# Kernel optimization log

Hardware: AMD Instinct MI355X
Metric: run time of the kernel (lower is better)

The kernel has to match this reference:

```python
import jax, jax.numpy as jnp
import numpy as np

B, G, NIN, H = 4, 1200, 10, 4
NHE, NINC = 300, 4800
ALPHA, BETA = 0.005, 5e-5
BN_EPS = 1e-5


def _linear_init(key, out_d, in_d):
    s = 1.0 / np.sqrt(in_d)
    kw, kb = jax.random.split(key)
    w = jax.random.uniform(kw, (out_d, in_d), jnp.float32, -s, s)
    b = jax.random.uniform(kb, (out_d,), jnp.float32, -s, s)
    return w, b


def setup_inputs() -> dict:
    key = jax.random.key(0)
    ks = jax.random.split(key, 16)
    d = {}
    d['x'] = jax.random.normal(ks[0], (B, G, NIN), jnp.float32)
    d['edge1'] = (jax.random.uniform(ks[1], (G, G)) < 0.02).astype(jnp.float32)
    d['edge2'] = (jax.random.uniform(ks[2], (G, G)) < 0.02).astype(jnp.float32)
    d['W1'] = jax.random.normal(ks[3], (G, G), jnp.float32) / np.sqrt(G)
    d['b1'] = jax.random.uniform(ks[4], (G,), jnp.float32)
    d['infer_w'], d['infer_b'] = _linear_init(ks[5], H, NIN)
    d['mlp_e1_w'], d['mlp_e1_b'] = _linear_init(ks[6], 1, 2 * H)
    d['mlp_e2_w'], d['mlp_e2_b'] = _linear_init(ks[7], 1, 2 * H)
    d['nodes1_w'], d['nodes1_b'] = _linear_init(ks[8], H, 2 * H)
    d['nodes2_w'], d['nodes2_b'] = _linear_init(ks[9], H, 2 * H)
    d['mm1_w'], d['mm1_b'] = _linear_init(ks[10], H, 2 * H)
    d['mm2_w'], d['mm2_b'] = _linear_init(ks[11], H, 2 * H)
    d['mm3_w'], d['mm3_b'] = _linear_init(ks[12], H, 2 * H)
    d['hg_w'], d['hg_b'] = _linear_init(ks[13], H, H)
    d['hyper_nodes'] = jax.random.randint(ks[14], (NINC,), 0, G)
    d['hyper_edges'] = jax.random.randint(ks[15], (NINC,), 0, NHE)
    return d


def _bn(y):
    # BatchNorm1d(gene_num) in train mode, gamma=1 beta=0: normalize per gene over (batch, feat)
    m = y.mean(axis=(0, 2), keepdims=True)
    v = y.var(axis=(0, 2), keepdims=True)
    return (y - m) * jax.lax.rsqrt(v + BN_EPS)


def _round(x, edge, coef, ew, eb, nw, nb, mw, mb):
    # one-hot matmul gather == repeat/tile; flat edge k = i*G + j, i=target, j=source
    Bsz, Gn, Hd = x.shape
    xi = jnp.repeat(x, Gn, axis=1)            # x[:, k // G]  (node_shape1 @ x)
    xj = jnp.tile(x, (1, Gn, 1))              # x[:, k %  G]  (node_shape2 @ x)
    ef = jnp.concatenate([xj, xi], axis=-1)   # [B, G*G, 2H]
    gate = jax.nn.sigmoid(ef @ ew.T + eb)     # [B, G*G, 1]
    mask = (edge + coef * (edge == 0).astype(x.dtype)).reshape(1, Gn * Gn, 1)
    msg = ef * (gate * mask)
    # transpose-matmul scatter back to target node i == sum over j
    recv = msg.reshape(Bsz, Gn, Gn, 2 * Hd).sum(axis=2)
    recv = jax.nn.elu(recv @ nw.T + nb)
    return jax.nn.elu(jnp.concatenate([recv, x], axis=-1) @ mw.T + mb)


def _forward(x, edge1, edge2, W1, b1, infer_w, infer_b, mlp_e1_w, mlp_e1_b,
             mlp_e2_w, mlp_e2_b, nodes1_w, nodes1_b, nodes2_w, nodes2_b,
             mm1_w, mm1_b, mm2_w, mm2_b, mm3_w, mm3_b, hg_w, hg_b,
             hyper_nodes, hyper_edges):
    Bsz, Gn, _ = x.shape
    h = jax.nn.elu(x @ infer_w.T + infer_b)                      # [B, G, H]
    upd = _round(h, edge1, ALPHA, mlp_e1_w, mlp_e1_b, nodes1_w, nodes1_b, mm1_w, mm1_b)
    # F.linear with w1 = eye(G) * W1 is a per-gene diagonal scale + per-gene bias
    h = jax.nn.elu(upd * jnp.diag(W1)[None, :, None] + b1[None, :, None])
    h = _bn(h)
    upd2 = _bn(_round(h, edge2, BETA, mlp_e2_w, mlp_e2_b, nodes2_w, nodes2_b, mm2_w, mm2_b))
    # HypergraphConv (PyG): out = D^-1 H (B^-1 H^T (X W)) + b.  Source overwrites the
    # hyper_graph1 result, so only hyper_graph2 contributes to the output.
    xf = upd2.reshape(Bsz * Gn, -1) @ hg_w.T
    node_idx = (hyper_nodes[None, :] + jnp.arange(Bsz)[:, None] * Gn).reshape(-1)
    edge_idx = jnp.tile(hyper_edges, Bsz)    # hyperedge ids NOT offset per batch (source quirk)
    nn_tot = Bsz * Gn
    ones = jnp.ones(node_idx.shape, xf.dtype)
    deg = jax.ops.segment_sum(ones, node_idx, num_segments=nn_tot)
    dinv = jnp.where(deg > 0, 1.0 / deg, 0.0)
    bdeg = jax.ops.segment_sum(ones, edge_idx, num_segments=NHE)
    binv = jnp.where(bdeg > 0, 1.0 / bdeg, 0.0)
    efeat = binv[:, None] * jax.ops.segment_sum(xf[node_idx], edge_idx, num_segments=NHE)
    hx = dinv[:, None] * jax.ops.segment_sum(efeat[edge_idx], node_idx, num_segments=nn_tot)
    hx = jax.nn.elu(hx + hg_b).reshape(Bsz, Gn, -1)
    return jax.nn.elu(jnp.concatenate([upd2, hx], axis=-1) @ mm3_w.T + mm3_b)


def reference(x, edge1, edge2, W1, b1, infer_w, infer_b, mlp_e1_w, mlp_e1_b,
              mlp_e2_w, mlp_e2_b, nodes1_w, nodes1_b, nodes2_w, nodes2_b,
              mm1_w, mm1_b, mm2_w, mm2_b, mm3_w, mm3_b, hg_w, hg_b,
              hyper_nodes, hyper_edges):
    return _forward(x, edge1, edge2, W1, b1, infer_w, infer_b, mlp_e1_w, mlp_e1_b,
                    mlp_e2_w, mlp_e2_b, nodes1_w, nodes1_b, nodes2_w, nodes2_b,
                    mm1_w, mm1_b, mm2_w, mm2_b, mm3_w, mm3_b, hg_w, hg_b,
                    hyper_nodes, hyper_edges)
```

## Files before the change

kernel.cpp:

```cpp
#include <hip/hip_runtime.h>
#include <math.h>

#define G 1200
#define BSZ 4
#define NIN 10
#define NHE 300
#define NINC 4800
#define ALPHA 0.005f
#define BETA 5e-5f
#define BN_EPS 1e-5f

__device__ __forceinline__ float eluf(float x) { return x > 0.f ? x : __expf(x) - 1.f; }
__device__ __forceinline__ float sigf(float x) { return 1.f / (1.f + __expf(-x)); }

__global__ __launch_bounds__(256)
void infer_kernel(const float* __restrict__ x,
                  const float* __restrict__ infer_w, const float* __restrict__ infer_b,
                  const float* __restrict__ e1w, const float* __restrict__ e1b,
                  float4* __restrict__ xfeat1, float* __restrict__ a1, float* __restrict__ c1,
                  int* __restrict__ zero_region ) {
    if (blockIdx.x == 0) {
        for (int t = threadIdx.x; t < NHE * 4 + NHE * 0 + 1200 + 300 - 1200; t += 256) {}
        for (int t = threadIdx.x; t < 1500; t += 256) zero_region[t] = 0;
    }
    int n = blockIdx.x * blockDim.x + threadIdx.x;
    if (n >= BSZ * G) return;
    const float* xp = x + n * NIN;
    float h[4];
#pragma unroll
    for (int f = 0; f < 4; ++f) {
        float s = infer_b[f];
#pragma unroll
        for (int k = 0; k < NIN; ++k) s += infer_w[f * NIN + k] * xp[k];
        h[f] = eluf(s);
    }
    xfeat1[n] = make_float4(h[0], h[1], h[2], h[3]);
    float av = 0.f, cv = 0.f;
#pragma unroll
    for (int f = 0; f < 4; ++f) { av += e1w[f] * h[f]; cv += e1w[4 + f] * h[f]; }
    a1[n] = av;
    c1[n] = cv + e1b[0];
}

template <int MODE>
__global__ __launch_bounds__(256)
void round_kernel(const float* __restrict__ edge, float coef,
                  const float4* __restrict__ xfeat,
                  const float* __restrict__ a, const float* __restrict__ c,
                  const float* __restrict__ nw, const float* __restrict__ nb,
                  const float* __restrict__ mw, const float* __restrict__ mb,
                  const float* __restrict__ W1, const float* __restrict__ b1,
                  const float* __restrict__ gw, const float* __restrict__ gb,
                  const float* __restrict__ hgw,
                  float4* __restrict__ out_feat,
                  float* __restrict__ a_out, float* __restrict__ c_out,
                  const int* __restrict__ hn, const int* __restrict__ he,
                  float* __restrict__ efeat_g, int* __restrict__ eh_g,
                  int* __restrict__ deg_g) {
    const int i = blockIdx.x;
    const int tid = threadIdx.x;
    const int lane = tid & 63;
    const int w = tid >> 6;
    const float* erow = edge + (size_t)i * G;

    const float cb = c[w * G + i];
    float acc0 = 0.f, acc1 = 0.f, acc2 = 0.f, acc3 = 0.f, acc4 = 0.f;

    for (int j = lane; j < G; j += 64) {
        float m = erow[j];
        float mask = (m == 0.f) ? coef : m;
        float4 xj = xfeat[w * G + j];
        float s = sigf(a[w * G + j] + cb) * mask;
        acc0 += s * xj.x;
        acc1 += s * xj.y;
        acc2 += s * xj.z;
        acc3 += s * xj.w;
        acc4 += s;
    }
#pragma unroll
    for (int o = 32; o > 0; o >>= 1) {
        acc0 += __shfl_down(acc0, o, 64);
        acc1 += __shfl_down(acc1, o, 64);
        acc2 += __shfl_down(acc2, o, 64);
        acc3 += __shfl_down(acc3, o, 64);
        acc4 += __shfl_down(acc4, o, 64);
    }

    __shared__ float t[4][5];
    __shared__ float hvs[4][4];
    __shared__ float stats[2];
    __shared__ float bss[4][4];
    __shared__ float bsf[4];
    __shared__ int degs;

    if (lane == 0) {
        t[w][0] = acc0; t[w][1] = acc1; t[w][2] = acc2; t[w][3] = acc3; t[w][4] = acc4;
    }
    if (tid == 0) degs = 0;
    __syncthreads();

    if (tid < 4) {
        const int b = tid;
        float4 xi4 = xfeat[b * G + i];
        float xi[4] = {xi4.x, xi4.y, xi4.z, xi4.w};
        float ssum = t[b][4];
        float r8[8];
#pragma unroll
        for (int k = 0; k < 4; ++k) { r8[k] = t[b][k]; r8[4 + k] = xi[k] * ssum; }
        float r[4];
#pragma unroll
        for (int f = 0; f < 4; ++f) {
            float s = nb[f];
#pragma unroll
            for (int k = 0; k < 8; ++k) s += nw[f * 8 + k] * r8[k];
            r[f] = eluf(s);
        }
        float w1d = 0.f, b1i = 0.f;
        if (MODE == 1) { w1d = W1[(size_t)i * G + i]; b1i = b1[i]; }
#pragma unroll
        for (int f = 0; f < 4; ++f) {
            float s = mb[f];
#pragma unroll
            for (int k = 0; k < 4; ++k) s += mw[f * 8 + k] * r[k] + mw[f * 8 + 4 + k] * xi[k];
            float z = eluf(s);
            hvs[b][f] = (MODE == 1) ? eluf(z * w1d + b1i) : z;
        }
    }
    __syncthreads();

    if (tid == 0) {
        float mean = 0.f;
#pragma unroll
        for (int b = 0; b < 4; ++b)
#pragma unroll
            for (int f = 0; f < 4; ++f) mean += hvs[b][f];
        mean *= (1.f / 16.f);
        float var = 0.f;
#pragma unroll
        for (int b = 0; b < 4; ++b)
#pragma unroll
            for (int f = 0; f < 4; ++f) { float d = hvs[b][f] - mean; var += d * d; }
        var *= (1.f / 16.f);
        stats[0] = mean;
        stats[1] = rsqrtf(var + BN_EPS);
    }
    __syncthreads();

    if (tid < 4) {
        const int b = tid;
        const float mean = stats[0], sc = stats[1];
        float hv[4];
#pragma unroll
        for (int f = 0; f < 4; ++f) hv[f] = (hvs[b][f] - mean) * sc;
        out_feat[b * G + i] = make_float4(hv[0], hv[1], hv[2], hv[3]);
        if (MODE == 1) {
            float av = 0.f, cv = 0.f;
#pragma unroll
            for (int f = 0; f < 4; ++f) { av += gw[f] * hv[f]; cv += gw[4 + f] * hv[f]; }
            a_out[b * G + i] = av;
            c_out[b * G + i] = cv + gb[0];
        } else {
#pragma unroll
            for (int f = 0; f < 4; ++f) {
                float s = 0.f;
#pragma unroll
                for (int k = 0; k < 4; ++k) s += hgw[f * 4 + k] * hv[k];
                bss[b][f] = s;
            }
        }
    }

    if (MODE == 2) {
        __syncthreads();
        if (tid < 4) bsf[tid] = bss[0][tid] + bss[1][tid] + bss[2][tid] + bss[3][tid];
        __syncthreads();
        const float b0 = bsf[0], b1v = bsf[1], b2 = bsf[2], b3 = bsf[3];
        int cnt = 0;
        for (int cI = tid; cI < NINC; cI += 256) {
            if (hn[cI] == i) {
                ++cnt;
                int e = he[cI];
                atomicAdd(&eh_g[e], 1);
                atomicAdd(&efeat_g[e * 4 + 0], b0);
                atomicAdd(&efeat_g[e * 4 + 1], b1v);
                atomicAdd(&efeat_g[e * 4 + 2], b2);
                atomicAdd(&efeat_g[e * 4 + 3], b3);
            }
        }
        if (cnt) atomicAdd(&degs, cnt);
        __syncthreads();
        if (tid == 0) deg_g[i] = degs;
    }
}

__global__ __launch_bounds__(256)
void final_kernel(const int* __restrict__ hn, const int* __restrict__ he,
                  const float* __restrict__ efeat_g, const int* __restrict__ eh_g,
                  const int* __restrict__ deg_g,
                  const float4* __restrict__ upd2, const float* __restrict__ hgb,
                  const float* __restrict__ m3w, const float* __restrict__ m3b,
                  float4* __restrict__ out) {
    const int i = blockIdx.x;
    const int tid = threadIdx.x;
    const int lane = tid & 63;
    const int w = tid >> 6;

    float a0 = 0.f, a1 = 0.f, a2 = 0.f, a3 = 0.f;
    for (int cI = tid; cI < NINC; cI += 256) {
        if (hn[cI] == i) {
            int e = he[cI];
            float binv = 0.25f / (float)eh_g[e];
            a0 += efeat_g[e * 4 + 0] * binv;
            a1 += efeat_g[e * 4 + 1] * binv;
            a2 += efeat_g[e * 4 + 2] * binv;
            a3 += efeat_g[e * 4 + 3] * binv;
        }
    }
#pragma unroll
    for (int o = 32; o > 0; o >>= 1) {
        a0 += __shfl_down(a0, o, 64);
        a1 += __shfl_down(a1, o, 64);
        a2 += __shfl_down(a2, o, 64);
        a3 += __shfl_down(a3, o, 64);
    }
    __shared__ float red[4][4];
    if (lane == 0) { red[w][0] = a0; red[w][1] = a1; red[w][2] = a2; red[w][3] = a3; }
    __syncthreads();

    if (tid < 4) {
        const int b = tid;
        int dg = deg_g[i];
        float dinv = dg > 0 ? 1.f / (float)dg : 0.f;
        float hxp[4];
#pragma unroll
        for (int f = 0; f < 4; ++f) {
            float hx = (red[0][f] + red[1][f] + red[2][f] + red[3][f]) * dinv;
            hxp[f] = eluf(hx + hgb[f]);
        }
        float4 u4 = upd2[b * G + i];
        float u[4] = {u4.x, u4.y, u4.z, u4.w};
        float o4[4];
#pragma unroll
        for (int f = 0; f < 4; ++f) {
            float s = m3b[f];
#pragma unroll
            for (int k = 0; k < 4; ++k) s += m3w[f * 8 + k] * u[k] + m3w[f * 8 + 4 + k] * hxp[k];
            o4[f] = eluf(s);
        }
        out[b * G + i] = make_float4(o4[0], o4[1], o4[2], o4[3]);
    }
}

extern "C" void kernel_launch(void* const* d_in, const int* in_sizes, int n_in,
                              void* d_out, int out_size, void* d_ws, size_t ws_size,
                              hipStream_t stream) {
    const float* x       = (const float*)d_in[0];
    const float* edge1   = (const float*)d_in[1];
    const float* edge2   = (const float*)d_in[2];
    const float* W1      = (const float*)d_in[3];
    const float* b1      = (const float*)d_in[4];
    const float* infer_w = (const float*)d_in[5];
    const float* infer_b = (const float*)d_in[6];
    const float* e1w     = (const float*)d_in[7];
    const float* e1b     = (const float*)d_in[8];
    const float* e2w     = (const float*)d_in[9];
    const float* e2b     = (const float*)d_in[10];
    const float* n1w     = (const float*)d_in[11];
    const float* n1b     = (const float*)d_in[12];
    const float* n2w     = (const float*)d_in[13];
    const float* n2b     = (const float*)d_in[14];
    const float* m1w     = (const float*)d_in[15];
    const float* m1b     = (const float*)d_in[16];
    const float* m2w     = (const float*)d_in[17];
    const float* m2b     = (const float*)d_in[18];
    const float* m3w     = (const float*)d_in[19];
    const float* m3b     = (const float*)d_in[20];
    const float* hgw     = (const float*)d_in[21];
    const float* hgb     = (const float*)d_in[22];
    const int*   hn      = (const int*)d_in[23];
    const int*   he      = (const int*)d_in[24];

    char* ws = (char*)d_ws;
    float4* xfeat1 = (float4*)(ws + 0);
    float4* xfeat2 = (float4*)(ws + 76800);
    float4* upd2   = (float4*)(ws + 153600);
    float*  a1     = (float*)(ws + 230400);
    float*  c1     = (float*)(ws + 249600);
    float*  a2     = (float*)(ws + 268800);
    float*  c2     = (float*)(ws + 288000);
    float*  efeat  = (float*)(ws + 307200);
    int*    eh     = (int*)(ws + 312000);
    int*    deg    = (int*)(ws + 313200);

    infer_kernel<<<(BSZ * G + 255) / 256, 256, 0, stream>>>(
        x, infer_w, infer_b, e1w, e1b, xfeat1, a1, c1, (int*)efeat);
    round_kernel<1><<<G, 256, 0, stream>>>(
        edge1, ALPHA, xfeat1, a1, c1, n1w, n1b, m1w, m1b, W1, b1, e2w, e2b, nullptr,
        xfeat2, a2, c2, nullptr, nullptr, nullptr, nullptr, nullptr);
    round_kernel<2><<<G, 256, 0, stream>>>(
        edge2, BETA, xfeat2, a2, c2, n2w, n2b, m2w, m2b, nullptr, nullptr, nullptr, nullptr, hgw,
        upd2, nullptr, nullptr, hn, he, efeat, eh, deg);
    final_kernel<<<G, 256, 0, stream>>>(
        hn, he, efeat, eh, deg, upd2, hgb, m3w, m3b, (float4*)d_out);
}
```

Before: 46.07 us.

## Fuse all stages into one cooperative kernel with grid syncs and LDS-staged features

Replaces the four separate launches with one cooperative kernel of 256 blocks × 1024 threads. Grid-wide syncs separate the infer/round1, round2 and final phases. Each block recomputes the full node feature and gate arrays into shared memory, so the per-edge loop reads LDS instead of global memory, and each block handles four nodes per pass. Node degree is now counted in the final phase instead of by atomics. The cost is redundant per-block recomputation of all 4800 features, about 96KB of LDS per block, grid-sync latency, and fewer concurrent waves, with a three-launch fallback if the cooperative launch fails.

```diff
diff --git a/kernel.cpp b/kernel.cpp
--- a/kernel.cpp
+++ b/kernel.cpp
@@ -1,305 +1,326 @@
 #include <hip/hip_runtime.h>
+#include <hip/hip_cooperative_groups.h>
 #include <math.h>
 
+namespace cg = cooperative_groups;
+
 #define G 1200
-#define BSZ 4
 #define NIN 10
 #define NHE 300
 #define NINC 4800
 #define ALPHA 0.005f
 #define BETA 5e-5f
 #define BN_EPS 1e-5f
+#define NBLK 256
+#define NTHR 1024
+
+struct Params {
+    const float *x, *edge1, *edge2, *W1, *b1, *infer_w, *infer_b;
+    const float *e1w, *e1b, *e2w, *e2b;
+    const float *n1w, *n1b, *n2w, *n2b;
+    const float *m1w, *m1b, *m2w, *m2b, *m3w, *m3b;
+    const float *hgw, *hgb;
+    const int *hn, *he;
+    float4 *xfeat2, *upd2;
+    float *efeat;
+    int *eh;
+    float4 *out;
+};
+
+struct Smem {
+    float4 h4[4 * G];
+    float  aarr[4 * G];
+    float  t[4][4][5];
+    float  hvs[4][4][4];
+    float  stats[4][2];
+    float  bsf[4][4];
+};
 
 __device__ __forceinline__ float eluf(float x) { return x > 0.f ? x : __expf(x) - 1.f; }
 __device__ __forceinline__ float sigf(float x) { return 1.f / (1.f + __expf(-x)); }
-
-__global__ __launch_bounds__(256)
-void infer_kernel(const float* __restrict__ x,
-                  const float* __restrict__ infer_w, const float* __restrict__ infer_b,
-                  const float* __restrict__ e1w, const float* __restrict__ e1b,
-                  float4* __restrict__ xfeat1, float* __restrict__ a1, float* __restrict__ c1,
-                  int* __restrict__ zero_region ) {
-    if (blockIdx.x == 0) {
-        for (int t = threadIdx.x; t < NHE * 4 + NHE * 0 + 1200 + 300 - 1200; t += 256) {}
-        for (int t = threadIdx.x; t < 1500; t += 256) zero_region[t] = 0;
-    }
-    int n = blockIdx.x * blockDim.x + threadIdx.x;
-    if (n >= BSZ * G) return;
-    const float* xp = x + n * NIN;
-    float h[4];
-#pragma unroll
-    for (int f = 0; f < 4; ++f) {
-        float s = infer_b[f];
-#pragma unroll
-        for (int k = 0; k < NIN; ++k) s += infer_w[f * NIN + k] * xp[k];
-        h[f] = eluf(s);
-    }
-    xfeat1[n] = make_float4(h[0], h[1], h[2], h[3]);
-    float av = 0.f, cv = 0.f;
-#pragma unroll
-    for (int f = 0; f < 4; ++f) { av += e1w[f] * h[f]; cv += e1w[4 + f] * h[f]; }
-    a1[n] = av;
-    c1[n] = cv + e1b[0];
+__device__ __forceinline__ float wred(float v) {
+#pragma unroll
+    for (int o = 32; o > 0; o >>= 1) v += __shfl_down(v, o, 64);
+    return v;
 }
 
 template <int MODE>
-__global__ __launch_bounds__(256)
-void round_kernel(const float* __restrict__ edge, float coef,
-                  const float4* __restrict__ xfeat,
-                  const float* __restrict__ a, const float* __restrict__ c,
-                  const float* __restrict__ nw, const float* __restrict__ nb,
-                  const float* __restrict__ mw, const float* __restrict__ mb,
-                  const float* __restrict__ W1, const float* __restrict__ b1,
-                  const float* __restrict__ gw, const float* __restrict__ gb,
-                  const float* __restrict__ hgw,
-                  float4* __restrict__ out_feat,
-                  float* __restrict__ a_out, float* __restrict__ c_out,
-                  const int* __restrict__ hn, const int* __restrict__ he,
-                  float* __restrict__ efeat_g, int* __restrict__ eh_g,
-                  int* __restrict__ deg_g) {
-    const int i = blockIdx.x;
-    const int tid = threadIdx.x;
+__device__ void round_phase(const Params& p, Smem& sm, int blk, int tid,
+                            const float* __restrict__ edge, float coef,
+                            const float* __restrict__ ew, const float* __restrict__ eb,
+                            const float* __restrict__ nw, const float* __restrict__ nb,
+                            const float* __restrict__ mw, const float* __restrict__ mb) {
     const int lane = tid & 63;
-    const int w = tid >> 6;
-    const float* erow = edge + (size_t)i * G;
-
-    const float cb = c[w * G + i];
-    float acc0 = 0.f, acc1 = 0.f, acc2 = 0.f, acc3 = 0.f, acc4 = 0.f;
-
-    for (int j = lane; j < G; j += 64) {
-        float m = erow[j];
-        float mask = (m == 0.f) ? coef : m;
-        float4 xj = xfeat[w * G + j];
-        float s = sigf(a[w * G + j] + cb) * mask;
-        acc0 += s * xj.x;
-        acc1 += s * xj.y;
-        acc2 += s * xj.z;
-        acc3 += s * xj.w;
-        acc4 += s;
-    }
-#pragma unroll
-    for (int o = 32; o > 0; o >>= 1) {
-        acc0 += __shfl_down(acc0, o, 64);
-        acc1 += __shfl_down(acc1, o, 64);
-        acc2 += __shfl_down(acc2, o, 64);
-        acc3 += __shfl_down(acc3, o, 64);
-        acc4 += __shfl_down(acc4, o, 64);
-    }
-
-    __shared__ float t[4][5];
-    __shared__ float hvs[4][4];
-    __shared__ float stats[2];
-    __shared__ float bss[4][4];
-    __shared__ float bsf[4];
-    __shared__ int degs;
-
-    if (lane == 0) {
-        t[w][0] = acc0; t[w][1] = acc1; t[w][2] = acc2; t[w][3] = acc3; t[w][4] = acc4;
-    }
-    if (tid == 0) degs = 0;
+    const int b = (tid >> 6) & 3;
+    const int slot = tid >> 8;
+    const int tslot = tid & 255;
+
+    for (int s = 0; s < 2; ++s) {
+        const int i = (s << 10) + (blk << 2) + slot;
+        const bool active = (i < G);
+
+        if (active) {
+            const float* erow = edge + (size_t)i * G;
+            float4 hi = sm.h4[b * G + i];
+            float cb = ew[4] * hi.x + ew[5] * hi.y + ew[6] * hi.z + ew[7] * hi.w + eb[0];
+            float a0 = 0.f, a1 = 0.f, a2 = 0.f, a3 = 0.f, a4 = 0.f;
+            for (int j = lane; j < G; j += 64) {
+                float m = erow[j];
+                float mask = (m == 0.f) ? coef : m;
+                float4 hj = sm.h4[b * G + j];
+                float sg = sigf(sm.aarr[b * G + j] + cb) * mask;
+                a0 += sg * hj.x;
+                a1 += sg * hj.y;
+                a2 += sg * hj.z;
+                a3 += sg * hj.w;
+                a4 += sg;
+            }
+            a0 = wred(a0); a1 = wred(a1); a2 = wred(a2); a3 = wred(a3); a4 = wred(a4);
+            if (lane == 0) {
+                sm.t[slot][b][0] = a0; sm.t[slot][b][1] = a1; sm.t[slot][b][2] = a2;
+                sm.t[slot][b][3] = a3; sm.t[slot][b][4] = a4;
+            }
+        }
+        __syncthreads();
+
+        if (active && lane == 0) {
+            float4 xi4 = sm.h4[b * G + i];
+            float xi[4] = {xi4.x, xi4.y, xi4.z, xi4.w};
+            float ssum = sm.t[slot][b][4];
+            float r8[8];
+#pragma unroll
+            for (int k = 0; k < 4; ++k) { r8[k] = sm.t[slot][b][k]; r8[4 + k] = xi[k] * ssum; }
+            float r[4];
+#pragma unroll
+            for (int f = 0; f < 4; ++f) {
+                float sv = nb[f];
+#pragma unroll
+                for (int k = 0; k < 8; ++k) sv += nw[f * 8 + k] * r8[k];
+                r[f] = eluf(sv);
+            }
+            float w1d = 0.f, b1i = 0.f;
+            if (MODE == 1) { w1d = p.W1[(size_t)i * G + i]; b1i = p.b1[i]; }
+#pragma unroll
+            for (int f = 0; f < 4; ++f) {
+                float sv = mb[f];
+#pragma unroll
+                for (int k = 0; k < 4; ++k) sv += mw[f * 8 + k] * r[k] + mw[f * 8 + 4 + k] * xi[k];
+                float z = eluf(sv);
+                sm.hvs[slot][b][f] = (MODE == 1) ? eluf(z * w1d + b1i) : z;
+            }
+        }
+        __syncthreads();
+
+        if (tslot == 0) {
+            float mean = 0.f;
+#pragma unroll
+            for (int bb = 0; bb < 4; ++bb)
+#pragma unroll
+                for (int f = 0; f < 4; ++f) mean += sm.hvs[slot][bb][f];
+            mean *= (1.f / 16.f);
+            float var = 0.f;
+#pragma unroll
+            for (int bb = 0; bb < 4; ++bb)
+#pragma unroll
+                for (int f = 0; f < 4; ++f) { float d = sm.hvs[slot][bb][f] - mean; var += d * d; }
+            var *= (1.f / 16.f);
+            sm.stats[slot][0] = mean;
+            sm.stats[slot][1] = rsqrtf(var + BN_EPS);
+        }
+        __syncthreads();
+
+        if (active && lane == 0) {
+            const float mean = sm.stats[slot][0], sc = sm.stats[slot][1];
+            float hv[4];
+#pragma unroll
+            for (int f = 0; f < 4; ++f) hv[f] = (sm.hvs[slot][b][f] - mean) * sc;
+            if (MODE == 1) {
+                p.xfeat2[b * G + i] = make_float4(hv[0], hv[1], hv[2], hv[3]);
+            } else {
+                p.upd2[b * G + i] = make_float4(hv[0], hv[1], hv[2], hv[3]);
+                sm.hvs[slot][b][0] = hv[0]; sm.hvs[slot][b][1] = hv[1];
+                sm.hvs[slot][b][2] = hv[2]; sm.hvs[slot][b][3] = hv[3];
+            }
+        }
+
+        if (MODE == 2) {
+            __syncthreads();
+            if (active && tslot < 4) {
+                const int f = tslot;
+                float sv = 0.f;
+#pragma unroll
+                for (int bb = 0; bb < 4; ++bb)
+#pragma unroll
+                    for (int k = 0; k < 4; ++k) sv += p.hgw[f * 4 + k] * sm.hvs[slot][bb][k];
+                sm.bsf[slot][f] = sv;
+            }
+            __syncthreads();
+            if (active) {
+                const float v0 = sm.bsf[slot][0], v1 = sm.bsf[slot][1];
+                const float v2 = sm.bsf[slot][2], v3 = sm.bsf[slot][3];
+                for (int cI = tslot; cI < NINC; cI += 256) {
+                    if (p.hn[cI] == i) {
+                        int e = p.he[cI];
+                        atomicAdd(&p.eh[e], 1);
+                        atomicAdd(&p.efeat[e * 4 + 0], v0);
+                        atomicAdd(&p.efeat[e * 4 + 1], v1);
+                        atomicAdd(&p.efeat[e * 4 + 2], v2);
+                        atomicAdd(&p.efeat[e * 4 + 3], v3);
+                    }
+                }
+            }
+        }
+        __syncthreads();
+    }
+}
+
+__device__ void phase1(const Params& p, Smem& sm, int blk, int tid) {
+    if (blk == 0) {
+        for (int q = tid; q < NHE * 4; q += NTHR) p.efeat[q] = 0.f;
+        for (int q = tid; q < NHE; q += NTHR) p.eh[q] = 0;
+    }
+    for (int n = tid; n < 4 * G; n += NTHR) {
+        const float* xp = p.x + n * NIN;
+        float h[4];
+#pragma unroll
+        for (int f = 0; f < 4; ++f) {
+            float sv = p.infer_b[f];
+#pragma unroll
+            for (int k = 0; k < NIN; ++k) sv += p.infer_w[f * NIN + k] * xp[k];
+            h[f] = eluf(sv);
+        }
+        sm.h4[n] = make_float4(h[0], h[1], h[2], h[3]);
+        sm.aarr[n] = p.e1w[0] * h[0] + p.e1w[1] * h[1] + p.e1w[2] * h[2] + p.e1w[3] * h[3];
+    }
     __syncthreads();
-
-    if (tid < 4) {
-        const int b = tid;
-        float4 xi4 = xfeat[b * G + i];
-        float xi[4] = {xi4.x, xi4.y, xi4.z, xi4.w};
-        float ssum = t[b][4];
-        float r8[8];
-#pragma unroll
-        for (int k = 0; k < 4; ++k) { r8[k] = t[b][k]; r8[4 + k] = xi[k] * ssum; }
-        float r[4];
-#pragma unroll
-        for (int f = 0; f < 4; ++f) {
-            float s = nb[f];
-#pragma unroll
-            for (int k = 0; k < 8; ++k) s += nw[f * 8 + k] * r8[k];
-            r[f] = eluf(s);
-        }
-        float w1d = 0.f, b1i = 0.f;
-        if (MODE == 1) { w1d = W1[(size_t)i * G + i]; b1i = b1[i]; }
-#pragma unroll
-        for (int f = 0; f < 4; ++f) {
-            float s = mb[f];
-#pragma unroll
-            for (int k = 0; k < 4; ++k) s += mw[f * 8 + k] * r[k] + mw[f * 8 + 4 + k] * xi[k];
-            float z = eluf(s);
-            hvs[b][f] = (MODE == 1) ? eluf(z * w1d + b1i) : z;
-        }
+    round_phase<1>(p, sm, blk, tid, p.edge1, ALPHA, p.e1w, p.e1b, p.n1w, p.n1b, p.m1w, p.m1b);
+}
+
+__device__ void phase2(const Params& p, Smem& sm, int blk, int tid) {
+    for (int n = tid; n < 4 * G; n += NTHR) {
+        float4 v = p.xfeat2[n];
+        sm.h4[n] = v;
+        sm.aarr[n] = p.e2w[0] * v.x + p.e2w[1] * v.y + p.e2w[2] * v.z + p.e2w[3] * v.w;
     }
     __syncthreads();
-
-    if (tid == 0) {
-        float mean = 0.f;
-#pragma unroll
-        for (int b = 0; b < 4; ++b)
-#pragma unroll
-            for (int f = 0; f < 4; ++f) mean += hvs[b][f];
-        mean *= (1.f / 16.f);
-        float var = 0.f;
-#pragma unroll
-        for (int b = 0; b < 4; ++b)
-#pragma unroll
-            for (int f = 0; f < 4; ++f) { float d = hvs[b][f] - mean; var += d * d; }
-        var *= (1.f / 16.f);
-        stats[0] = mean;
-        stats[1] = rsqrtf(var + BN_EPS);
-    }
-    __syncthreads();
-
-    if (tid < 4) {
-        const int b = tid;
-        const float mean = stats[0], sc = stats[1];
-        float hv[4];
-#pragma unroll
-        for (int f = 0; f < 4; ++f) hv[f] = (hvs[b][f] - mean) * sc;
-        out_feat[b * G + i] = make_float4(hv[0], hv[1], hv[2], hv[3]);
-        if (MODE == 1) {
-            float av = 0.f, cv = 0.f;
-#pragma unroll
-            for (int f = 0; f < 4; ++f) { av += gw[f] * hv[f]; cv += gw[4 + f] * hv[f]; }
-            a_out[b * G + i] = av;
-            c_out[b * G + i] = cv + gb[0];
-        } else {
+    round_phase<2>(p, sm, blk, tid, p.edge2, BETA, p.e2w, p.e2b, p.n2w, p.n2b, p.m2w, p.m2b);
+}
+
+__device__ void phase3(const Params& p, Smem& sm, int blk, int tid) {
+    const int lane = tid & 63;
+    const int b = (tid >> 6) & 3;
+    const int slot = tid >> 8;
+    const int tslot = tid & 255;
+
+    for (int s = 0; s < 2; ++s) {
+        const int i = (s << 10) + (blk << 2) + slot;
+        const bool active = (i < G);
+        float a0 = 0.f, a1 = 0.f, a2 = 0.f, a3 = 0.f, cf = 0.f;
+        if (active) {
+            for (int cI = tslot; cI < NINC; cI += 256) {
+                if (p.hn[cI] == i) {
+                    int e = p.he[cI];
+                    float binv = 0.25f / (float)p.eh[e];
+                    a0 += p.efeat[e * 4 + 0] * binv;
+                    a1 += p.efeat[e * 4 + 1] * binv;
+                    a2 += p.efeat[e * 4 + 2] * binv;
+                    a3 += p.efeat[e * 4 + 3] * binv;
+                    cf += 1.f;
+                }
+            }
+        }
+        a0 = wred(a0); a1 = wred(a1); a2 = wred(a2); a3 = wred(a3); cf = wred(cf);
+        if (lane == 0) {
+            sm.t[slot][b][0] = a0; sm.t[slot][b][1] = a1; sm.t[slot][b][2] = a2;
+            sm.t[slot][b][3] = a3; sm.t[slot][b][4] = cf;
+        }
+        __syncthreads();
+
+        if (active && lane == 0) {
+            float dg = sm.t[slot][0][4] + sm.t[slot][1][4] + sm.t[slot][2][4] + sm.t[slot][3][4];
+            float dinv = dg > 0.f ? 1.f / dg : 0.f;
+            float hxp[4];
 #pragma unroll
             for (int f = 0; f < 4; ++f) {
-                float s = 0.f;
-#pragma unroll
-                for (int k = 0; k < 4; ++k) s += hgw[f * 4 + k] * hv[k];
-                bss[b][f] = s;
-            }
-        }
-    }
-
-    if (MODE == 2) {
-        __syncthreads();
-        if (tid < 4) bsf[tid] = bss[0][tid] + bss[1][tid] + bss[2][tid] + bss[3][tid];
-        __syncthreads();
-        const float b0 = bsf[0], b1v = bsf[1], b2 = bsf[2], b3 = bsf[3];
-        int cnt = 0;
-        for (int cI = tid; cI < NINC; cI += 256) {
-            if (hn[cI] == i) {
-                ++cnt;
-                int e = he[cI];
-                atomicAdd(&eh_g[e], 1);
-                atomicAdd(&efeat_g[e * 4 + 0], b0);
-                atomicAdd(&efeat_g[e * 4 + 1], b1v);
-                atomicAdd(&efeat_g[e * 4 + 2], b2);
-                atomicAdd(&efeat_g[e * 4 + 3], b3);
-            }
-        }
-        if (cnt) atomicAdd(&degs, cnt);
-        __syncthreads();
-        if (tid == 0) deg_g[i] = degs;
-    }
-}
-
-__global__ __launch_bounds__(256)
-void final_kernel(const int* __restrict__ hn, const int* __restrict__ he,
-                  const float* __restrict__ efeat_g, const int* __restrict__ eh_g,
-                  const int* __restrict__ deg_g,
-                  const float4* __restrict__ upd2, const float* __restrict__ hgb,
-                  const float* __restrict__ m3w, const float* __restrict__ m3b,
-                  float4* __restrict__ out) {
-    const int i = blockIdx.x;
-    const int tid = threadIdx.x;
-    const int lane = tid & 63;
-    const int w = tid >> 6;
-
-    float a0 = 0.f, a1 = 0.f, a2 = 0.f, a3 = 0.f;
-    for (int cI = tid; cI < NINC; cI += 256) {
-        if (hn[cI] == i) {
-            int e = he[cI];
-            float binv = 0.25f / (float)eh_g[e];
-            a0 += efeat_g[e * 4 + 0] * binv;
-            a1 += efeat_g[e * 4 + 1] * binv;
-            a2 += efeat_g[e * 4 + 2] * binv;
-            a3 += efeat_g[e * 4 + 3] * binv;
-        }
-    }
-#pragma unroll
-    for (int o = 32; o > 0; o >>= 1) {
-        a0 += __shfl_down(a0, o, 64);
-        a1 += __shfl_down(a1, o, 64);
-        a2 += __shfl_down(a2, o, 64);
-        a3 += __shfl_down(a3, o, 64);
-    }
-    __shared__ float red[4][4];
-    if (lane == 0) { red[w][0] = a0; red[w][1] = a1; red[w][2] = a2; red[w][3] = a3; }
-    __syncthreads();
-
-    if (tid < 4) {
-        const int b = tid;
-        int dg = deg_g[i];
-        float dinv = dg > 0 ? 1.f / (float)dg : 0.f;
-        float hxp[4];
-#pragma unroll
-        for (int f = 0; f < 4; ++f) {
-            float hx = (red[0][f] + red[1][f] + red[2][f] + red[3][f]) * dinv;
-            hxp[f] = eluf(hx + hgb[f]);
-        }
-        float4 u4 = upd2[b * G + i];
-        float u[4] = {u4.x, u4.y, u4.z, u4.w};
-        float o4[4];
-#pragma unroll
-        for (int f = 0; f < 4; ++f) {
-            float s = m3b[f];
-#pragma unroll
-            for (int k = 0; k < 4; ++k) s += m3w[f * 8 + k] * u[k] + m3w[f * 8 + 4 + k] * hxp[k];
-            o4[f] = eluf(s);
-        }
-        out[b * G + i] = make_float4(o4[0], o4[1], o4[2], o4[3]);
-    }
-}
+                float hx = (sm.t[slot][0][f] + sm.t[slot][1][f] + sm.t[slot][2][f] +
+                            sm.t[slot][3][f]) * dinv;
+                hxp[f] = eluf(hx + p.hgb[f]);
+            }
+            float4 u4 = p.upd2[b * G + i];
+            float u[4] = {u4.x, u4.y, u4.z, u4.w};
+            float o4[4];
+#pragma unroll
+            for (int f = 0; f < 4; ++f) {
+                float sv = p.m3b[f];
+#pragma unroll
+                for (int k = 0; k < 4; ++k)
+                    sv += p.m3w[f * 8 + k] * u[k] + p.m3w[f * 8 + 4 + k] * hxp[k];
+                o4[f] = eluf(sv);
+            }
+            p.out[b * G + i] = make_float4(o4[0], o4[1], o4[2], o4[3]);
+        }
+        __syncthreads();
+    }
+}
+
+__global__ __launch_bounds__(NTHR)
+void fused_kernel(Params p) {
+    __shared__ Smem sm;
+    cg::grid_group grid = cg::this_grid();
+    phase1(p, sm, blockIdx.x, threadIdx.x);
+    grid.sync();
+    phase2(p, sm, blockIdx.x, threadIdx.x);
+    grid.sync();
+    phase3(p, sm, blockIdx.x, threadIdx.x);
+}
+
+__global__ __launch_bounds__(NTHR) void k_p1(Params p) { __shared__ Smem sm; phase1(p, sm, blockIdx.x, threadIdx.x); }
+__global__ __launch_bounds__(NTHR) void k_p2(Params p) { __shared__ Smem sm; phase2(p, sm, blockIdx.x, threadIdx.x); }
+__global__ __launch_bounds__(NTHR) void k_p3(Params p) { __shared__ Smem sm; phase3(p, sm, blockIdx.x, threadIdx.x); }
 
 extern "C" void kernel_launch(void* const* d_in, const int* in_sizes, int n_in,
                               void* d_out, int out_size, void* d_ws, size_t ws_size,
                               hipStream_t stream) {
-    const float* x       = (const float*)d_in[0];
-    const float* edge1   = (const float*)d_in[1];
-    const float* edge2   = (const float*)d_in[2];
-    const float* W1      = (const float*)d_in[3];
-    const float* b1      = (const float*)d_in[4];
-    const float* infer_w = (const float*)d_in[5];
-    const float* infer_b = (const float*)d_in[6];
-    const float* e1w     = (const float*)d_in[7];
-    const float* e1b     = (const float*)d_in[8];
-    const float* e2w     = (const float*)d_in[9];
-    const float* e2b     = (const float*)d_in[10];
-    const float* n1w     = (const float*)d_in[11];
-    const float* n1b     = (const float*)d_in[12];
-    const float* n2w     = (const float*)d_in[13];
-    const float* n2b     = (const float*)d_in[14];
-    const float* m1w     = (const float*)d_in[15];
-    const float* m1b     = (const float*)d_in[16];
-    const float* m2w     = (const float*)d_in[17];
-    const float* m2b     = (const float*)d_in[18];
-    const float* m3w     = (const float*)d_in[19];
-    const float* m3b     = (const float*)d_in[20];
-    const float* hgw     = (const float*)d_in[21];
-    const float* hgb     = (const float*)d_in[22];
-    const int*   hn      = (const int*)d_in[23];
-    const int*   he      = (const int*)d_in[24];
+    Params p;
+    p.x       = (const float*)d_in[0];
+    p.edge1   = (const float*)d_in[1];
+    p.edge2   = (const float*)d_in[2];
+    p.W1      = (const float*)d_in[3];
+    p.b1      = (const float*)d_in[4];
+    p.infer_w = (const float*)d_in[5];
+    p.infer_b = (const float*)d_in[6];
+    p.e1w     = (const float*)d_in[7];
+    p.e1b     = (const float*)d_in[8];
+    p.e2w     = (const float*)d_in[9];
+    p.e2b     = (const float*)d_in[10];
+    p.n1w     = (const float*)d_in[11];
+    p.n1b     = (const float*)d_in[12];
+    p.n2w     = (const float*)d_in[13];
+    p.n2b     = (const float*)d_in[14];
+    p.m1w     = (const float*)d_in[15];
+    p.m1b     = (const float*)d_in[16];
+    p.m2w     = (const float*)d_in[17];
+    p.m2b     = (const float*)d_in[18];
+    p.m3w     = (const float*)d_in[19];
+    p.m3b     = (const float*)d_in[20];
+    p.hgw     = (const float*)d_in[21];
+    p.hgb     = (const float*)d_in[22];
+    p.hn      = (const int*)d_in[23];
+    p.he      = (const int*)d_in[24];
 
     char* ws = (char*)d_ws;
-    float4* xfeat1 = (float4*)(ws + 0);
-    float4* xfeat2 = (float4*)(ws + 76800);
-    float4* upd2   = (float4*)(ws + 153600);
-    float*  a1     = (float*)(ws + 230400);
-    float*  c1     = (float*)(ws + 249600);
-    float*  a2     = (float*)(ws + 268800);
-    float*  c2     = (float*)(ws + 288000);
-    float*  efeat  = (float*)(ws + 307200);
-    int*    eh     = (int*)(ws + 312000);
-    int*    deg    = (int*)(ws + 313200);
-
-    infer_kernel<<<(BSZ * G + 255) / 256, 256, 0, stream>>>(
-        x, infer_w, infer_b, e1w, e1b, xfeat1, a1, c1, (int*)efeat);
-    round_kernel<1><<<G, 256, 0, stream>>>(
-        edge1, ALPHA, xfeat1, a1, c1, n1w, n1b, m1w, m1b, W1, b1, e2w, e2b, nullptr,
-        xfeat2, a2, c2, nullptr, nullptr, nullptr, nullptr, nullptr);
-    round_kernel<2><<<G, 256, 0, stream>>>(
-        edge2, BETA, xfeat2, a2, c2, n2w, n2b, m2w, m2b, nullptr, nullptr, nullptr, nullptr, hgw,
-        upd2, nullptr, nullptr, hn, he, efeat, eh, deg);
-    final_kernel<<<G, 256, 0, stream>>>(
-        hn, he, efeat, eh, deg, upd2, hgb, m3w, m3b, (float4*)d_out);
-}
+    p.xfeat2 = (float4*)(ws + 0);
+    p.upd2   = (float4*)(ws + 76800);
+    p.efeat  = (float*)(ws + 153600);
+    p.eh     = (int*)(ws + 158400);
+    p.out    = (float4*)d_out;
+
+    void* args[] = {(void*)&p};
+    hipError_t err = hipLaunchCooperativeKernel((const void*)fused_kernel,
+                                                dim3(NBLK), dim3(NTHR), args, 0, stream);
+    if (err != hipSuccess) {
+        k_p1<<<NBLK, NTHR, 0, stream>>>(p);
+        k_p2<<<NBLK, NTHR, 0, stream>>>(p);
+        k_p3<<<NBLK, NTHR, 0, stream>>>(p);
+    }
+}
```

After: 129.1 us. 180% more time.

## Fuse infer into round1, move hypergraph scatter into final kernel via LDS

Applied to the files above, without the earlier changes.

Removes the separate infer kernel. Round-1 blocks recompute the inferred node features on the fly from x, and each block handles two target rows so the features are reused. The round-2 kernel now loads the edge rows and a-values as float4 and writes per-node hypergraph contributions without global atomics. The final kernel rebuilds the per-edge sums in shared memory with LDS atomics and computes node degrees itself. This saves a launch and removes global atomics and zeroing, at the cost of redundant feature recompute in round 1 and redundant full-incidence scatter in every final block.

```diff
diff --git a/kernel.cpp b/kernel.cpp
--- a/kernel.cpp
+++ b/kernel.cpp
@@ -2,7 +2,6 @@
 #include <math.h>
 
 #define G 1200
-#define BSZ 4
 #define NIN 10
 #define NHE 300
 #define NINC 4800
@@ -12,96 +11,197 @@
 
 __device__ __forceinline__ float eluf(float x) { return x > 0.f ? x : __expf(x) - 1.f; }
 __device__ __forceinline__ float sigf(float x) { return 1.f / (1.f + __expf(-x)); }
+__device__ __forceinline__ float wred(float v) {
+#pragma unroll
+    for (int o = 32; o > 0; o >>= 1) v += __shfl_down(v, o, 64);
+    return v;
+}
+__device__ __forceinline__ float maskf(float e, float coef) { return (e == 0.f) ? coef : e; }
 
 __global__ __launch_bounds__(256)
-void infer_kernel(const float* __restrict__ x,
-                  const float* __restrict__ infer_w, const float* __restrict__ infer_b,
-                  const float* __restrict__ e1w, const float* __restrict__ e1b,
-                  float4* __restrict__ xfeat1, float* __restrict__ a1, float* __restrict__ c1,
-                  int* __restrict__ zero_region ) {
-    if (blockIdx.x == 0) {
-        for (int t = threadIdx.x; t < NHE * 4 + NHE * 0 + 1200 + 300 - 1200; t += 256) {}
-        for (int t = threadIdx.x; t < 1500; t += 256) zero_region[t] = 0;
-    }
-    int n = blockIdx.x * blockDim.x + threadIdx.x;
-    if (n >= BSZ * G) return;
-    const float* xp = x + n * NIN;
-    float h[4];
-#pragma unroll
-    for (int f = 0; f < 4; ++f) {
-        float s = infer_b[f];
-#pragma unroll
-        for (int k = 0; k < NIN; ++k) s += infer_w[f * NIN + k] * xp[k];
-        h[f] = eluf(s);
-    }
-    xfeat1[n] = make_float4(h[0], h[1], h[2], h[3]);
-    float av = 0.f, cv = 0.f;
-#pragma unroll
-    for (int f = 0; f < 4; ++f) { av += e1w[f] * h[f]; cv += e1w[4 + f] * h[f]; }
-    a1[n] = av;
-    c1[n] = cv + e1b[0];
-}
-
-template <int MODE>
+void k_round1(const float* __restrict__ x,
+              const float* __restrict__ edge1,
+              const float* __restrict__ W1, const float* __restrict__ b1,
+              const float* __restrict__ iw, const float* __restrict__ ib,
+              const float* __restrict__ e1w, const float* __restrict__ e1b,
+              const float* __restrict__ n1w, const float* __restrict__ n1b,
+              const float* __restrict__ m1w, const float* __restrict__ m1b,
+              const float* __restrict__ e2w, const float* __restrict__ e2b,
+              float4* __restrict__ xfeat2, float* __restrict__ a2, float* __restrict__ c2) {
+    const int tid = threadIdx.x;
+    const int lane = tid & 63;
+    const int w = tid >> 6;
+    const int i0 = blockIdx.x, i1 = blockIdx.x + 600;
+
+    float hi0[4], hi1[4];
+    {
+        const float* xp0 = x + ((size_t)w * G + i0) * NIN;
+        const float* xp1 = x + ((size_t)w * G + i1) * NIN;
+#pragma unroll
+        for (int f = 0; f < 4; ++f) {
+            float s0 = ib[f], s1 = ib[f];
+#pragma unroll
+            for (int k = 0; k < NIN; ++k) { s0 += iw[f * NIN + k] * xp0[k]; s1 += iw[f * NIN + k] * xp1[k]; }
+            hi0[f] = eluf(s0);
+            hi1[f] = eluf(s1);
+        }
+    }
+    const float cb0 = e1w[4] * hi0[0] + e1w[5] * hi0[1] + e1w[6] * hi0[2] + e1w[7] * hi0[3] + e1b[0];
+    const float cb1 = e1w[4] * hi1[0] + e1w[5] * hi1[1] + e1w[6] * hi1[2] + e1w[7] * hi1[3] + e1b[0];
+
+    const float4* r0 = (const float4*)(edge1 + (size_t)i0 * G);
+    const float4* r1 = (const float4*)(edge1 + (size_t)i1 * G);
+
+    float acc[10];
+#pragma unroll
+    for (int k = 0; k < 10; ++k) acc[k] = 0.f;
+
+    for (int m = lane; m < 300; m += 64) {
+        float e0a[4], e1a[4];
+        *(float4*)e0a = r0[m];
+        *(float4*)e1a = r1[m];
+        float xf[40];
+        const float* xp = x + ((size_t)w * G + 4 * m) * NIN;
+#pragma unroll
+        for (int q = 0; q < 10; ++q) *(float4*)&xf[4 * q] = ((const float4*)xp)[q];
+#pragma unroll
+        for (int s = 0; s < 4; ++s) {
+            float h[4];
+#pragma unroll
+            for (int f = 0; f < 4; ++f) {
+                float sv = ib[f];
+#pragma unroll
+                for (int k = 0; k < NIN; ++k) sv += iw[f * NIN + k] * xf[10 * s + k];
+                h[f] = eluf(sv);
+            }
+            float aj = e1w[0] * h[0] + e1w[1] * h[1] + e1w[2] * h[2] + e1w[3] * h[3];
+            float sg0 = sigf(aj + cb0) * maskf(e0a[s], ALPHA);
+            float sg1 = sigf(aj + cb1) * maskf(e1a[s], ALPHA);
+            acc[0] += sg0 * h[0]; acc[1] += sg0 * h[1]; acc[2] += sg0 * h[2];
+            acc[3] += sg0 * h[3]; acc[4] += sg0;
+            acc[5] += sg1 * h[0]; acc[6] += sg1 * h[1]; acc[7] += sg1 * h[2];
+            acc[8] += sg1 * h[3]; acc[9] += sg1;
+        }
+    }
+#pragma unroll
+    for (int k = 0; k < 10; ++k) acc[k] = wred(acc[k]);
+
+    __shared__ float t[2][4][5];
+    __shared__ float him[2][4][4];
+    __shared__ float hvs[2][4][4];
+    __shared__ float stats[2][2];
+
+    if (lane == 0) {
+#pragma unroll
+        for (int k = 0; k < 5; ++k) { t[0][w][k] = acc[k]; t[1][w][k] = acc[5 + k]; }
+#pragma unroll
+        for (int f = 0; f < 4; ++f) { him[0][w][f] = hi0[f]; him[1][w][f] = hi1[f]; }
+    }
+    __syncthreads();
+
+    if (tid < 8) {
+        const int b = tid & 3, g = tid >> 2;
+        const int i = (g == 0) ? i0 : i1;
+        float xi[4] = {him[g][b][0], him[g][b][1], him[g][b][2], him[g][b][3]};
+        float ssum = t[g][b][4];
+        float r8[8];
+#pragma unroll
+        for (int k = 0; k < 4; ++k) { r8[k] = t[g][b][k]; r8[4 + k] = xi[k] * ssum; }
+        float r[4];
+#pragma unroll
+        for (int f = 0; f < 4; ++f) {
+            float sv = n1b[f];
+#pragma unroll
+            for (int k = 0; k < 8; ++k) sv += n1w[f * 8 + k] * r8[k];
+            r[f] = eluf(sv);
+        }
+        const float w1d = W1[(size_t)i * G + i], b1i = b1[i];
+#pragma unroll
+        for (int f = 0; f < 4; ++f) {
+            float sv = m1b[f];
+#pragma unroll
+            for (int k = 0; k < 4; ++k) sv += m1w[f * 8 + k] * r[k] + m1w[f * 8 + 4 + k] * xi[k];
+            hvs[g][b][f] = eluf(eluf(sv) * w1d + b1i);
+        }
+    }
+    __syncthreads();
+
+    if (tid < 2) {
+        const int g = tid;
+        float mean = 0.f;
+#pragma unroll
+        for (int bb = 0; bb < 4; ++bb)
+#pragma unroll
+            for (int f = 0; f < 4; ++f) mean += hvs[g][bb][f];
+        mean *= (1.f / 16.f);
+        float var = 0.f;
+#pragma unroll
+        for (int bb = 0; bb < 4; ++bb)
+#pragma unroll
+            for (int f = 0; f < 4; ++f) { float d = hvs[g][bb][f] - mean; var += d * d; }
+        var *= (1.f / 16.f);
+        stats[g][0] = mean;
+        stats[g][1] = rsqrtf(var + BN_EPS);
+    }
+    __syncthreads();
+
+    if (tid < 8) {
+        const int b = tid & 3, g = tid >> 2;
+        const int i = (g == 0) ? i0 : i1;
+        const float mean = stats[g][0], sc = stats[g][1];
+        float hv[4];
+#pragma unroll
+        for (int f = 0; f < 4; ++f) hv[f] = (hvs[g][b][f] - mean) * sc;
+        xfeat2[b * G + i] = make_float4(hv[0], hv[1], hv[2], hv[3]);
+        a2[b * G + i] = e2w[0] * hv[0] + e2w[1] * hv[1] + e2w[2] * hv[2] + e2w[3] * hv[3];
+        c2[b * G + i] = e2w[4] * hv[0] + e2w[5] * hv[1] + e2w[6] * hv[2] + e2w[7] * hv[3] + e2b[0];
+    }
+}
+
 __global__ __launch_bounds__(256)
-void round_kernel(const float* __restrict__ edge, float coef,
-                  const float4* __restrict__ xfeat,
-                  const float* __restrict__ a, const float* __restrict__ c,
-                  const float* __restrict__ nw, const float* __restrict__ nb,
-                  const float* __restrict__ mw, const float* __restrict__ mb,
-                  const float* __restrict__ W1, const float* __restrict__ b1,
-                  const float* __restrict__ gw, const float* __restrict__ gb,
-                  const float* __restrict__ hgw,
-                  float4* __restrict__ out_feat,
-                  float* __restrict__ a_out, float* __restrict__ c_out,
-                  const int* __restrict__ hn, const int* __restrict__ he,
-                  float* __restrict__ efeat_g, int* __restrict__ eh_g,
-                  int* __restrict__ deg_g) {
+void k_round2(const float* __restrict__ edge2,
+              const float4* __restrict__ xfeat2,
+              const float* __restrict__ a2, const float* __restrict__ c2,
+              const float* __restrict__ n2w, const float* __restrict__ n2b,
+              const float* __restrict__ m2w, const float* __restrict__ m2b,
+              const float* __restrict__ hgw,
+              float4* __restrict__ upd2, float* __restrict__ bs) {
     const int i = blockIdx.x;
     const int tid = threadIdx.x;
     const int lane = tid & 63;
     const int w = tid >> 6;
-    const float* erow = edge + (size_t)i * G;
-
-    const float cb = c[w * G + i];
+
+    const float cb = c2[w * G + i];
+    const float4* erow4 = (const float4*)(edge2 + (size_t)i * G);
+    const float4* a4 = (const float4*)(a2 + (size_t)w * G);
+
     float acc0 = 0.f, acc1 = 0.f, acc2 = 0.f, acc3 = 0.f, acc4 = 0.f;
-
-    for (int j = lane; j < G; j += 64) {
-        float m = erow[j];
-        float mask = (m == 0.f) ? coef : m;
-        float4 xj = xfeat[w * G + j];
-        float s = sigf(a[w * G + j] + cb) * mask;
-        acc0 += s * xj.x;
-        acc1 += s * xj.y;
-        acc2 += s * xj.z;
-        acc3 += s * xj.w;
-        acc4 += s;
-    }
-#pragma unroll
-    for (int o = 32; o > 0; o >>= 1) {
-        acc0 += __shfl_down(acc0, o, 64);
-        acc1 += __shfl_down(acc1, o, 64);
-        acc2 += __shfl_down(acc2, o, 64);
-        acc3 += __shfl_down(acc3, o, 64);
-        acc4 += __shfl_down(acc4, o, 64);
-    }
+    for (int m = lane; m < 300; m += 64) {
+        float ea[4], aa[4];
+        *(float4*)ea = erow4[m];
+        *(float4*)aa = a4[m];
+#pragma unroll
+        for (int s = 0; s < 4; ++s) {
+            float4 xv = xfeat2[w * G + 4 * m + s];
+            float sg = sigf(aa[s] + cb) * maskf(ea[s], BETA);
+            acc0 += sg * xv.x;
+            acc1 += sg * xv.y;
+            acc2 += sg * xv.z;
+            acc3 += sg * xv.w;
+            acc4 += sg;
+        }
+    }
+    acc0 = wred(acc0); acc1 = wred(acc1); acc2 = wred(acc2); acc3 = wred(acc3); acc4 = wred(acc4);
 
     __shared__ float t[4][5];
     __shared__ float hvs[4][4];
     __shared__ float stats[2];
-    __shared__ float bss[4][4];
-    __shared__ float bsf[4];
-    __shared__ int degs;
-
-    if (lane == 0) {
-        t[w][0] = acc0; t[w][1] = acc1; t[w][2] = acc2; t[w][3] = acc3; t[w][4] = acc4;
-    }
-    if (tid == 0) degs = 0;
+    if (lane == 0) { t[w][0] = acc0; t[w][1] = acc1; t[w][2] = acc2; t[w][3] = acc3; t[w][4] = acc4; }
     __syncthreads();
 
     if (tid < 4) {
         const int b = tid;
-        float4 xi4 = xfeat[b * G + i];
+        float4 xi4 = xfeat2[b * G + i];
         float xi[4] = {xi4.x, xi4.y, xi4.z, xi4.w};
         float ssum = t[b][4];
         float r8[8];
@@ -110,20 +210,17 @@
         float r[4];
 #pragma unroll
         for (int f = 0; f < 4; ++f) {
-            float s = nb[f];
-#pragma unroll
-            for (int k = 0; k < 8; ++k) s += nw[f * 8 + k] * r8[k];
-            r[f] = eluf(s);
-        }
-        float w1d = 0.f, b1i = 0.f;
-        if (MODE == 1) { w1d = W1[(size_t)i * G + i]; b1i = b1[i]; }
-#pragma unroll
-        for (int f = 0; f < 4; ++f) {
-            float s = mb[f];
-#pragma unroll
-            for (int k = 0; k < 4; ++k) s += mw[f * 8 + k] * r[k] + mw[f * 8 + 4 + k] * xi[k];
-            float z = eluf(s);
-            hvs[b][f] = (MODE == 1) ? eluf(z * w1d + b1i) : z;
+            float sv = n2b[f];
+#pragma unroll
+            for (int k = 0; k < 8; ++k) sv += n2w[f * 8 + k] * r8[k];
+            r[f] = eluf(sv);
+        }
+#pragma unroll
+        for (int f = 0; f < 4; ++f) {
+            float sv = m2b[f];
+#pragma unroll
+            for (int k = 0; k < 4; ++k) sv += m2w[f * 8 + k] * r[k] + m2w[f * 8 + 4 + k] * xi[k];
+            hvs[b][f] = eluf(sv);
         }
     }
     __syncthreads();
@@ -131,15 +228,15 @@
     if (tid == 0) {
         float mean = 0.f;
 #pragma unroll
-        for (int b = 0; b < 4; ++b)
-#pragma unroll
-            for (int f = 0; f < 4; ++f) mean += hvs[b][f];
+        for (int bb = 0; bb < 4; ++bb)
+#pragma unroll
+            for (int f = 0; f < 4; ++f) mean += hvs[bb][f];
         mean *= (1.f / 16.f);
         float var = 0.f;
 #pragma unroll
-        for (int b = 0; b < 4; ++b)
-#pragma unroll
-            for (int f = 0; f < 4; ++f) { float d = hvs[b][f] - mean; var += d * d; }
+        for (int bb = 0; bb < 4; ++bb)
+#pragma unroll
+            for (int f = 0; f < 4; ++f) { float d = hvs[bb][f] - mean; var += d * d; }
         var *= (1.f / 16.f);
         stats[0] = mean;
         stats[1] = rsqrtf(var + BN_EPS);
@@ -152,85 +249,75 @@
         float hv[4];
 #pragma unroll
         for (int f = 0; f < 4; ++f) hv[f] = (hvs[b][f] - mean) * sc;
-        out_feat[b * G + i] = make_float4(hv[0], hv[1], hv[2], hv[3]);
-        if (MODE == 1) {
-            float av = 0.f, cv = 0.f;
-#pragma unroll
-            for (int f = 0; f < 4; ++f) { av += gw[f] * hv[f]; cv += gw[4 + f] * hv[f]; }
-            a_out[b * G + i] = av;
-            c_out[b * G + i] = cv + gb[0];
-        } else {
-#pragma unroll
-            for (int f = 0; f < 4; ++f) {
-                float s = 0.f;
-#pragma unroll
-                for (int k = 0; k < 4; ++k) s += hgw[f * 4 + k] * hv[k];
-                bss[b][f] = s;
-            }
-        }
-    }
-
-    if (MODE == 2) {
-        __syncthreads();
-        if (tid < 4) bsf[tid] = bss[0][tid] + bss[1][tid] + bss[2][tid] + bss[3][tid];
-        __syncthreads();
-        const float b0 = bsf[0], b1v = bsf[1], b2 = bsf[2], b3 = bsf[3];
-        int cnt = 0;
-        for (int cI = tid; cI < NINC; cI += 256) {
-            if (hn[cI] == i) {
-                ++cnt;
-                int e = he[cI];
-                atomicAdd(&eh_g[e], 1);
-                atomicAdd(&efeat_g[e * 4 + 0], b0);
-                atomicAdd(&efeat_g[e * 4 + 1], b1v);
-                atomicAdd(&efeat_g[e * 4 + 2], b2);
-                atomicAdd(&efeat_g[e * 4 + 3], b3);
-            }
-        }
-        if (cnt) atomicAdd(&degs, cnt);
-        __syncthreads();
-        if (tid == 0) deg_g[i] = degs;
+        upd2[b * G + i] = make_float4(hv[0], hv[1], hv[2], hv[3]);
+        hvs[b][0] = hv[0]; hvs[b][1] = hv[1]; hvs[b][2] = hv[2]; hvs[b][3] = hv[3];
+    }
+    __syncthreads();
+
+    if (tid < 4) {
+        const int f = tid;
+        float sv = 0.f;
+#pragma unroll
+        for (int bb = 0; bb < 4; ++bb)
+#pragma unroll
+            for (int k = 0; k < 4; ++k) sv += hgw[f * 4 + k] * hvs[bb][k];
+        bs[i * 4 + f] = sv;
     }
 }
 
 __global__ __launch_bounds__(256)
-void final_kernel(const int* __restrict__ hn, const int* __restrict__ he,
-                  const float* __restrict__ efeat_g, const int* __restrict__ eh_g,
-                  const int* __restrict__ deg_g,
-                  const float4* __restrict__ upd2, const float* __restrict__ hgb,
-                  const float* __restrict__ m3w, const float* __restrict__ m3b,
-                  float4* __restrict__ out) {
+void k_final(const int* __restrict__ hn, const int* __restrict__ he,
+             const float* __restrict__ bs,
+             const float4* __restrict__ upd2, const float* __restrict__ hgb,
+             const float* __restrict__ m3w, const float* __restrict__ m3b,
+             float4* __restrict__ out) {
     const int i = blockIdx.x;
     const int tid = threadIdx.x;
     const int lane = tid & 63;
     const int w = tid >> 6;
 
-    float a0 = 0.f, a1 = 0.f, a2 = 0.f, a3 = 0.f;
+    __shared__ float ef[NHE][4];
+    __shared__ int eh[NHE];
+    __shared__ float red[4][5];
+
+    for (int t = tid; t < NHE; t += 256) {
+        eh[t] = 0;
+        ef[t][0] = ef[t][1] = ef[t][2] = ef[t][3] = 0.f;
+    }
+    __syncthreads();
+
+    const float4* bs4 = (const float4*)bs;
+    for (int cI = tid; cI < NINC; cI += 256) {
+        int n = hn[cI], e = he[cI];
+        float4 bv = bs4[n];
+        atomicAdd(&eh[e], 1);
+        atomicAdd(&ef[e][0], bv.x);
+        atomicAdd(&ef[e][1], bv.y);
+        atomicAdd(&ef[e][2], bv.z);
+        atomicAdd(&ef[e][3], bv.w);
+    }
+    __syncthreads();
+
+    float a0 = 0.f, a1 = 0.f, a2 = 0.f, a3 = 0.f, cf = 0.f;
     for (int cI = tid; cI < NINC; cI += 256) {
         if (hn[cI] == i) {
             int e = he[cI];
-            float binv = 0.25f / (float)eh_g[e];
-            a0 += efeat_g[e * 4 + 0] * binv;
-            a1 += efeat_g[e * 4 + 1] * binv;
-            a2 += efeat_g[e * 4 + 2] * binv;
-            a3 += efeat_g[e * 4 + 3] * binv;
-        }
-    }
-#pragma unroll
-    for (int o = 32; o > 0; o >>= 1) {
-        a0 += __shfl_down(a0, o, 64);
-        a1 += __shfl_down(a1, o, 64);
-        a2 += __shfl_down(a2, o, 64);
-        a3 += __shfl_down(a3, o, 64);
-    }
-    __shared__ float red[4][4];
-    if (lane == 0) { red[w][0] = a0; red[w][1] = a1; red[w][2] = a2; red[w][3] = a3; }
+            float binv = 0.25f / (float)eh[e];
+            a0 += ef[e][0] * binv;
+            a1 += ef[e][1] * binv;
+            a2 += ef[e][2] * binv;
+            a3 += ef[e][3] * binv;
+            cf += 1.f;
+        }
+    }
+    a0 = wred(a0); a1 = wred(a1); a2 = wred(a2); a3 = wred(a3); cf = wred(cf);
+    if (lane == 0) { red[w][0] = a0; red[w][1] = a1; red[w][2] = a2; red[w][3] = a3; red[w][4] = cf; }
     __syncthreads();
 
     if (tid < 4) {
         const int b = tid;
-        int dg = deg_g[i];
-        float dinv = dg > 0 ? 1.f / (float)dg : 0.f;
+        float dg = red[0][4] + red[1][4] + red[2][4] + red[3][4];
+        float dinv = dg > 0.f ? 1.f / dg : 0.f;
         float hxp[4];
 #pragma unroll
         for (int f = 0; f < 4; ++f) {
@@ -242,10 +329,11 @@
         float o4[4];
 #pragma unroll
         for (int f = 0; f < 4; ++f) {
-            float s = m3b[f];
-#pragma unroll
-            for (int k = 0; k < 4; ++k) s += m3w[f * 8 + k] * u[k] + m3w[f * 8 + 4 + k] * hxp[k];
-            o4[f] = eluf(s);
+            float sv = m3b[f];
+#pragma unroll
+            for (int k = 0; k < 4; ++k)
+                sv += m3w[f * 8 + k] * u[k] + m3w[f * 8 + 4 + k] * hxp[k];
+            o4[f] = eluf(sv);
         }
         out[b * G + i] = make_float4(o4[0], o4[1], o4[2], o4[3]);
     }
@@ -281,25 +369,15 @@
     const int*   he      = (const int*)d_in[24];
 
     char* ws = (char*)d_ws;
-    float4* xfeat1 = (float4*)(ws + 0);
-    float4* xfeat2 = (float4*)(ws + 76800);
-    float4* upd2   = (float4*)(ws + 153600);
-    float*  a1     = (float*)(ws + 230400);
-    float*  c1     = (float*)(ws + 249600);
-    float*  a2     = (float*)(ws + 268800);
-    float*  c2     = (float*)(ws + 288000);
-    float*  efeat  = (float*)(ws + 307200);
-    int*    eh     = (int*)(ws + 312000);
-    int*    deg    = (int*)(ws + 313200);
-
-    infer_kernel<<<(BSZ * G + 255) / 256, 256, 0, stream>>>(
-        x, infer_w, infer_b, e1w, e1b, xfeat1, a1, c1, (int*)efeat);
-    round_kernel<1><<<G, 256, 0, stream>>>(
-        edge1, ALPHA, xfeat1, a1, c1, n1w, n1b, m1w, m1b, W1, b1, e2w, e2b, nullptr,
-        xfeat2, a2, c2, nullptr, nullptr, nullptr, nullptr, nullptr);
-    round_kernel<2><<<G, 256, 0, stream>>>(
-        edge2, BETA, xfeat2, a2, c2, n2w, n2b, m2w, m2b, nullptr, nullptr, nullptr, nullptr, hgw,
-        upd2, nullptr, nullptr, hn, he, efeat, eh, deg);
-    final_kernel<<<G, 256, 0, stream>>>(
-        hn, he, efeat, eh, deg, upd2, hgb, m3w, m3b, (float4*)d_out);
-}
+    float4* xfeat2 = (float4*)(ws + 0);
+    float4* upd2   = (float4*)(ws + 76800);
+    float*  a2     = (float*)(ws + 153600);
+    float*  c2     = (float*)(ws + 172800);
+    float*  bs     = (float*)(ws + 192000);
+
+    k_round1<<<600, 256, 0, stream>>>(x, edge1, W1, b1, infer_w, infer_b, e1w, e1b,
+                                      n1w, n1b, m1w, m1b, e2w, e2b, xfeat2, a2, c2);
+    k_round2<<<1200, 256, 0, stream>>>(edge2, xfeat2, a2, c2, n2w, n2b, m2w, m2b, hgw,
+                                       upd2, bs);
+    k_final<<<1200, 256, 0, stream>>>(hn, he, bs, upd2, hgb, m3w, m3b, (float4*)d_out);
+}
```

Result: slower. 162.0 us (+251.6%).
